# Optimization experiments

Hardware: AMD Instinct MI355X
Metric: run time of the kernel (lower is better)

The kernel has to match this reference:

```python
import jax, jax.numpy as jnp
import numpy as np

N = 32768      # nodes
E = 524288     # edges (avg degree 16)
G = 512        # graphs in batch
F_IN = 64      # one-hot node-label dim
H = 128        # hidden_dim
C = 2          # num_classes (NCI1)
BN_EPS = 1e-3  # keras BatchNormalization default epsilon


def setup_inputs() -> dict:
    key = jax.random.key(0)
    ks = jax.random.split(key, 32)
    d = {}
    d["x"] = jax.random.normal(ks[0], (N, F_IN), jnp.float32)
    d["edge_weight"] = jax.random.uniform(ks[1], (E,), jnp.float32)
    i = 2
    din = F_IN
    for l in range(5):
        d[f"W1_{l}"] = jax.random.normal(ks[i], (din, H), jnp.float32) / np.float32(np.sqrt(din)); i += 1
        d[f"b1_{l}"] = jnp.zeros((H,), jnp.float32)
        d[f"W2_{l}"] = jax.random.normal(ks[i], (H, H), jnp.float32) / np.float32(np.sqrt(H)); i += 1
        d[f"b2_{l}"] = jnp.zeros((H,), jnp.float32)
        din = H
    for j in (1, 2, 3):  # bn1, bn2, bn3 (bn0/bn4 unused in original call())
        d[f"g{j}"] = jnp.ones((H,), jnp.float32)
        d[f"be{j}"] = jnp.zeros((H,), jnp.float32)
        d[f"m{j}"] = jnp.zeros((H,), jnp.float32)
        d[f"v{j}"] = jnp.ones((H,), jnp.float32)
    d["Wm1"] = jax.random.normal(ks[i], (5 * H, 128), jnp.float32) / np.float32(np.sqrt(5 * H)); i += 1
    d["bm1"] = jnp.zeros((128,), jnp.float32)
    d["Wm2"] = jax.random.normal(ks[i], (128, C), jnp.float32) / np.float32(np.sqrt(128.0)); i += 1
    d["bm2"] = jnp.zeros((C,), jnp.float32)
    d["edge_index"] = jax.random.randint(ks[i], (2, E), 0, N, dtype=jnp.int32); i += 1
    d["node_graph_index"] = jnp.sort(jax.random.randint(ks[i], (N,), 0, G, dtype=jnp.int32))
    return d


def reference(x, edge_weight,
              W1_0, b1_0, W2_0, b2_0,
              W1_1, b1_1, W2_1, b2_1,
              W1_2, b1_2, W2_2, b2_2,
              W1_3, b1_3, W2_3, b2_3,
              W1_4, b1_4, W2_4, b2_4,
              g1, be1, m1, v1,
              g2, be2, m2, v2,
              g3, be3, m3, v3,
              Wm1, bm1, Wm2, bm2,
              edge_index, node_graph_index):
    src, dst = edge_index[0], edge_index[1]

    def gin(h, W1, b1, W2, b2):
        # GIN with eps=0: h' = MLP(h + sum_{j in N(i)} w_ij * h_j)
        msg = h[dst] * edge_weight[:, None]              # [E, d]
        agg = jax.ops.segment_sum(msg, src, num_segments=N)
        h2 = h + agg
        return jax.nn.relu(h2 @ W1 + b1) @ W2 + b2

    def bn(h, g, be, m, v):  # inference-mode batchnorm
        return (h - m) * jax.lax.rsqrt(v + BN_EPS) * g + be

    h1 = gin(x, W1_0, b1_0, W2_0, b2_0)
    h2 = gin(bn(h1, g1, be1, m1, v1), W1_1, b1_1, W2_1, b2_1)
    h3 = gin(bn(h2, g1, be1, m1, v1), W1_2, b1_2, W2_2, b2_2)  # bn1 reused, as in source
    h4 = gin(bn(h3, g2, be2, m2, v2), W1_3, b1_3, W2_3, b2_3)
    h5 = gin(bn(h4, g3, be3, m3, v3), W1_4, b1_4, W2_4, b2_4)
    h5 = bn(h5, g3, be3, m3, v3)                                # bn3 reused, as in source

    pool = lambda h: jax.ops.segment_sum(h, node_graph_index, num_segments=G)
    hg = jnp.concatenate([pool(h1), pool(h2), pool(h3), pool(h4), pool(h5)], axis=-1)  # [G, 5H]
    # readout MLP (dropout inactive at inference)
    return jax.nn.relu(hg @ Wm1 + bm1) @ Wm2 + bm2  # [G, C]
```

## Files before the change

### kernel.cpp

```cpp
#include <hip/hip_runtime.h>
#include <hip/hip_bf16.h>

#define NN 32768
#define EE 524288
#define GG 512
#define CAP 48

typedef __bf16 bf16x8 __attribute__((ext_vector_type(8)));
typedef float  f32x4  __attribute__((ext_vector_type(4)));
typedef float  f32x2  __attribute__((ext_vector_type(2)));

#define F8_ENC 0.25f
#define F8_DEC 4.0f

static __device__ __forceinline__ float bf2f(unsigned short u) {
    union { unsigned int i; float f; } v; v.i = ((unsigned int)u) << 16; return v.f;
}
static __device__ __forceinline__ unsigned short f2bf(float f) {
    __bf16 b = (__bf16)f;
    return __builtin_bit_cast(unsigned short, b);
}
static __device__ __forceinline__ unsigned int pk2(float a, float b) {
    return (unsigned int)f2bf(a) | ((unsigned int)f2bf(b) << 16);
}
static __device__ __forceinline__ void fmaV4(float* a, float w, uint2 hv) {
    a[0] += w * bf2f((unsigned short)(hv.x & 0xffff));
    a[1] += w * bf2f((unsigned short)(hv.x >> 16));
    a[2] += w * bf2f((unsigned short)(hv.y & 0xffff));
    a[3] += w * bf2f((unsigned short)(hv.y >> 16));
}
static __device__ __forceinline__ void fmaV8f8(float* a, float w, uint2 hv) {
    f32x2 p;
    p = __builtin_amdgcn_cvt_pk_f32_fp8((int)hv.x, false); a[0] += w * p[0]; a[1] += w * p[1];
    p = __builtin_amdgcn_cvt_pk_f32_fp8((int)hv.x, true);  a[2] += w * p[0]; a[3] += w * p[1];
    p = __builtin_amdgcn_cvt_pk_f32_fp8((int)hv.y, false); a[4] += w * p[0]; a[5] += w * p[1];
    p = __builtin_amdgcn_cvt_pk_f32_fp8((int)hv.y, true);  a[6] += w * p[0]; a[7] += w * p[1];
}

struct WJob { const float* in; unsigned short* out; int K; };
struct WJobs { WJob j[10]; };

__global__ __launch_bounds__(256) void build_kernel(WJobs jobs,
                                                    const int* __restrict__ src,
                                                    const int* __restrict__ dst,
                                                    const float* __restrict__ w,
                                                    int* __restrict__ cnt,
                                                    unsigned int* __restrict__ csr,
                                                    const float* __restrict__ x,
                                                    unsigned short* __restrict__ xb) {
    if (blockIdx.x < 2048) {
        int e = blockIdx.x * 256 + threadIdx.x;
        int s = src[e];
        int slot = atomicAdd(&cnt[s], 1);
        if (slot < CAP)
            csr[(size_t)s * CAP + slot] = (unsigned int)dst[e] | ((unsigned int)f2bf(w[e]) << 16);
    } else if (blockIdx.x < 2088) {
        int b = blockIdx.x - 2048;
        WJob jb = jobs.j[b >> 2];
        int quarter = b & 3;
        int per = jb.K * 128 / 4;
        for (int idx = quarter * per + threadIdx.x; idx < (quarter + 1) * per; idx += 256) {
            int k = idx >> 7, c = idx & 127;
            jb.out[c * jb.K + k] = f2bf(jb.in[idx]);
        }
    } else {
        int base = (blockIdx.x - 2088) * 4096 + threadIdx.x;
        #pragma unroll
        for (int k = 0; k < 16; ++k) {
            int idx = base + k * 256;
            xb[idx] = f2bf(x[idx]);
        }
    }
}

template<bool FIRST>
__global__ __launch_bounds__(256, 8) void agg_kernel(
        const unsigned short* __restrict__ h_in,
        const unsigned char* __restrict__ h8_in,
        const int* __restrict__ cnt,
        const unsigned int* __restrict__ csr,
        unsigned short* __restrict__ A1g) {

    constexpr int CH = FIRST ? 4 : 8;

    int tid = threadIdx.x;
    int wave = tid >> 6, lane = tid & 63;
    int i4 = lane >> 4;
    int half = (lane >> 3) & 1;
    int sub8 = lane & 7;
    int gbase = lane & 56;
    int r = wave * 4 + i4;
    int node = blockIdx.x * 16 + r;
    int nb = blockIdx.x * 16 + wave * 4;

    int d0 = min(cnt[nb], CAP), d1 = min(cnt[nb + 1], CAP);
    int d2 = min(cnt[nb + 2], CAP), d3 = min(cnt[nb + 3], CAP);
    int deg = (i4 == 0) ? d0 : (i4 == 1) ? d1 : (i4 == 2) ? d2 : d3;
    int md = max(max(d0, d1), max(d2, d3));
    int mc = (md + 7) >> 3;
    size_t ebase = (size_t)node * CAP;
    int off = half * 8 + sub8;

    unsigned int ev[6];
    #pragma unroll
    for (int c = 0; c < 6; ++c) {
        int p = c * 8 + sub8;
        unsigned int e2 = 0;
        if (p < deg) e2 = csr[ebase + p];
        ev[c] = e2;
    }

    float acc[CH];
    #pragma unroll
    for (int c = 0; c < CH; ++c) acc[c] = 0.f;

    const uint2* hp = FIRST ? (const uint2*)h_in : (const uint2*)h8_in;

    uint2 pre[4]; float wv[4];
    #pragma unroll
    for (int k = 0; k < 4; ++k) {
        unsigned int e2 = (unsigned int)__shfl((int)ev[0], gbase | k);
        wv[k] = bf2f((unsigned short)(e2 >> 16));
        pre[k] = hp[(size_t)(e2 & 0xffffu) * 16 + off];
    }
    #pragma unroll
    for (int c = 0; c < 6; ++c) {
        if (c >= mc) break;
        #pragma unroll
        for (int j = 0; j < 8; ++j) {
            int t = c * 8 + j;
            if constexpr (FIRST) fmaV4(acc, wv[t & 3], pre[t & 3]);
            else                 fmaV8f8(acc, wv[t & 3], pre[t & 3]);
            int tn = t + 4, cn = tn >> 3, jn = tn & 7;
            if (cn < 6) {
                unsigned int e2 = (unsigned int)__shfl((int)ev[cn], gbase | jn);
                wv[t & 3] = bf2f((unsigned short)(e2 >> 16));
                pre[t & 3] = hp[(size_t)(e2 & 0xffffu) * 16 + off];
            }
        }
    }

    if constexpr (FIRST) {
        uint2 selfv = ((const uint2*)h_in)[(size_t)node * 16 + off];
        acc[0] += bf2f((unsigned short)(selfv.x & 0xffff));
        acc[1] += bf2f((unsigned short)(selfv.x >> 16));
        acc[2] += bf2f((unsigned short)(selfv.y & 0xffff));
        acc[3] += bf2f((unsigned short)(selfv.y >> 16));
        *(uint2*)(A1g + (size_t)node * 64 + off * 4) =
            make_uint2(pk2(acc[0], acc[1]), pk2(acc[2], acc[3]));
    } else {
        #pragma unroll
        for (int i = 0; i < 8; ++i) acc[i] *= F8_DEC;
        uint4 selfv = ((const uint4*)h_in)[(size_t)node * 16 + off];
        acc[0] += bf2f((unsigned short)(selfv.x & 0xffff));
        acc[1] += bf2f((unsigned short)(selfv.x >> 16));
        acc[2] += bf2f((unsigned short)(selfv.y & 0xffff));
        acc[3] += bf2f((unsigned short)(selfv.y >> 16));
        acc[4] += bf2f((unsigned short)(selfv.z & 0xffff));
        acc[5] += bf2f((unsigned short)(selfv.z >> 16));
        acc[6] += bf2f((unsigned short)(selfv.w & 0xffff));
        acc[7] += bf2f((unsigned short)(selfv.w >> 16));
        *(uint4*)(A1g + (size_t)node * 128 + off * 8) =
            make_uint4(pk2(acc[0], acc[1]), pk2(acc[2], acc[3]),
                       pk2(acc[4], acc[5]), pk2(acc[6], acc[7]));
    }
}

template<bool FIRST, bool LAST>
__global__ __launch_bounds__(256) void mlp_kernel(
        const unsigned short* __restrict__ A1g,
        const unsigned short* __restrict__ W1t,
        const float* __restrict__ b1,
        const unsigned short* __restrict__ W2t,
        const float* __restrict__ b2,
        const float* __restrict__ g, const float* __restrict__ be,
        const float* __restrict__ m, const float* __restrict__ v,
        const int* __restrict__ gidx,
        unsigned short* __restrict__ h_out,
        unsigned char* __restrict__ h8_out,
        float* __restrict__ pools, int col_off) {

    constexpr int K1 = FIRST ? 64 : 128;
    constexpr int KS1 = K1 / 32;

    __shared__ unsigned int smem[2176];
    __shared__ float sscale[128], sshift[128];
    __shared__ int sgid[16];

    unsigned int* A1 = smem;
    unsigned int* T  = smem + 16 * 68;
    float* OUT = (float*)smem;

    int tid = threadIdx.x;
    int wave = tid >> 6, lane = tid & 63;
    int mrow = lane & 15, quad = lane >> 4;

    if (tid < 128) {
        float sc = g[tid] * rsqrtf(v[tid] + 1e-3f);
        sscale[tid] = sc;
        sshift[tid] = be[tid] - m[tid] * sc;
    } else if (tid < 144) {
        sgid[tid - 128] = gidx[blockIdx.x * 16 + (tid - 128)];
    }

    unsigned short* A1s = (unsigned short*)A1;
    if constexpr (FIRST) {
        if (tid < 128) {
            int row = tid >> 3, grp = tid & 7;
            *(uint4*)(A1s + row * 136 + grp * 8) =
                *(const uint4*)(A1g + (size_t)(blockIdx.x * 16 + row) * 64 + grp * 8);
        }
    } else {
        int row = tid >> 4, grp = tid & 15;
        *(uint4*)(A1s + row * 136 + grp * 8) =
            *(const uint4*)(A1g + (size_t)(blockIdx.x * 16 + row) * 128 + grp * 8);
    }
    __syncthreads();

    unsigned short* Ts = (unsigned short*)T;

    bf16x8 af[KS1];
    #pragma unroll
    for (int kk = 0; kk < KS1; ++kk)
        af[kk] = *(const bf16x8*)(A1s + mrow * 136 + kk * 32 + quad * 8);

    f32x4 acc1v[2];
    #pragma unroll
    for (int c = 0; c < 2; ++c) acc1v[c] = (f32x4){0.f, 0.f, 0.f, 0.f};
    #pragma unroll
    for (int c = 0; c < 2; ++c) {
        const bf16x8* Brow = (const bf16x8*)(W1t + (size_t)(wave * 32 + c * 16 + mrow) * K1);
        #pragma unroll
        for (int kk = 0; kk < KS1; ++kk)
            acc1v[c] = __builtin_amdgcn_mfma_f32_16x16x32_bf16(af[kk], Brow[kk * 4 + quad], acc1v[c], 0, 0, 0);
    }
    #pragma unroll
    for (int c = 0; c < 2; ++c) {
        int ocol = wave * 32 + c * 16 + mrow;
        float bv = b1[ocol];
        #pragma unroll
        for (int r = 0; r < 4; ++r)
            Ts[(quad * 4 + r) * 136 + ocol] = f2bf(fmaxf(acc1v[c][r] + bv, 0.f));
    }
    __syncthreads();

    bf16x8 a2f[4];
    #pragma unroll
    for (int kk = 0; kk < 4; ++kk)
        a2f[kk] = *(const bf16x8*)(Ts + mrow * 136 + kk * 32 + quad * 8);
    f32x4 acc2v[2];
    #pragma unroll
    for (int c = 0; c < 2; ++c) acc2v[c] = (f32x4){0.f, 0.f, 0.f, 0.f};
    #pragma unroll
    for (int c = 0; c < 2; ++c) {
        const bf16x8* Brow = (const bf16x8*)(W2t + (size_t)(wave * 32 + c * 16 + mrow) * 128);
        #pragma unroll
        for (int kk = 0; kk < 4; ++kk)
            acc2v[c] = __builtin_amdgcn_mfma_f32_16x16x32_bf16(a2f[kk], Brow[kk * 4 + quad], acc2v[c], 0, 0, 0);
    }
    __syncthreads();

    #pragma unroll
    for (int c = 0; c < 2; ++c) {
        int ocol = wave * 32 + c * 16 + mrow;
        float bv = b2[ocol];
        #pragma unroll
        for (int r = 0; r < 4; ++r)
            OUT[(quad * 4 + r) * 132 + ocol] = acc2v[c][r] + bv;
    }
    __syncthreads();

    if (!LAST) {
        int row = tid >> 4, q = tid & 15;
        const float* Op = OUT + row * 132 + q * 8;
        float o[8];
        #pragma unroll
        for (int i = 0; i < 8; ++i) {
            int c = q * 8 + i;
            o[i] = Op[i] * sscale[c] + sshift[c];
        }
        size_t rowbase = (size_t)(blockIdx.x * 16 + row);
        *(uint4*)(h_out + rowbase * 128 + q * 8) =
            make_uint4(pk2(o[0], o[1]), pk2(o[2], o[3]),
                       pk2(o[4], o[5]), pk2(o[6], o[7]));
        int w0 = __builtin_amdgcn_cvt_pk_fp8_f32(o[0] * F8_ENC, o[1] * F8_ENC, 0, false);
        w0 = __builtin_amdgcn_cvt_pk_fp8_f32(o[2] * F8_ENC, o[3] * F8_ENC, w0, true);
        int w1 = __builtin_amdgcn_cvt_pk_fp8_f32(o[4] * F8_ENC, o[5] * F8_ENC, 0, false);
        w1 = __builtin_amdgcn_cvt_pk_fp8_f32(o[6] * F8_ENC, o[7] * F8_ENC, w1, true);
        *(uint2*)(h8_out + rowbase * 128 + q * 8) =
            make_uint2((unsigned int)w0, (unsigned int)w1);
    }

    {
        int col = tid & 127, half = tid >> 7;
        float sc = LAST ? sscale[col] : 1.f;
        float sh = LAST ? sshift[col] : 0.f;
        float accp = 0.f;
        int cur = sgid[half * 8];
        for (int r = half * 8; r < half * 8 + 8; ++r) {
            int gi = sgid[r];
            if (gi != cur) {
                atomicAdd(&pools[(size_t)cur * 640 + col_off + col], accp);
                accp = 0.f;
                cur = gi;
            }
            float val = OUT[r * 132 + col];
            accp += LAST ? (val * sc + sh) : val;
        }
        atomicAdd(&pools[(size_t)cur * 640 + col_off + col], accp);
    }
}

__global__ __launch_bounds__(128) void readout(const float* __restrict__ pools,
                                               const float* __restrict__ Wm1,
                                               const float* __restrict__ bm1,
                                               const float* __restrict__ Wm2,
                                               const float* __restrict__ bm2,
                                               float* __restrict__ out) {
    __shared__ float row[640];
    __shared__ float partial[4];
    int gb = blockIdx.x;
    for (int k = threadIdx.x; k < 640; k += 128) row[k] = pools[(size_t)gb * 640 + k];
    __syncthreads();
    int j = threadIdx.x;
    float acc = bm1[j];
    for (int k = 0; k < 640; ++k) acc += row[k] * Wm1[(size_t)k * 128 + j];
    acc = fmaxf(acc, 0.f);
    float p0 = acc * Wm2[j * 2], p1 = acc * Wm2[j * 2 + 1];
    #pragma unroll
    for (int off = 32; off; off >>= 1) { p0 += __shfl_down(p0, off); p1 += __shfl_down(p1, off); }
    int wave = j >> 6;
    if ((j & 63) == 0) { partial[wave * 2] = p0; partial[wave * 2 + 1] = p1; }
    __syncthreads();
    if (j == 0) {
        out[gb * 2]     = bm2[0] + partial[0] + partial[2];
        out[gb * 2 + 1] = bm2[1] + partial[1] + partial[3];
    }
}

extern "C" void kernel_launch(void* const* d_in, const int* in_sizes, int n_in,
                              void* d_out, int out_size, void* d_ws, size_t ws_size,
                              hipStream_t stream) {
    const float* x  = (const float*)d_in[0];
    const float* ew = (const float*)d_in[1];
    const float *W1[5], *b1[5], *W2[5], *b2[5];
    for (int l = 0; l < 5; ++l) {
        W1[l] = (const float*)d_in[2 + 4 * l];
        b1[l] = (const float*)d_in[3 + 4 * l];
        W2[l] = (const float*)d_in[4 + 4 * l];
        b2[l] = (const float*)d_in[5 + 4 * l];
    }
    const float *bg[3], *bb[3], *bm[3], *bv[3];
    for (int j = 0; j < 3; ++j) {
        bg[j] = (const float*)d_in[22 + 4 * j];
        bb[j] = (const float*)d_in[23 + 4 * j];
        bm[j] = (const float*)d_in[24 + 4 * j];
        bv[j] = (const float*)d_in[25 + 4 * j];
    }
    const float* Wm1 = (const float*)d_in[34];
    const float* bm1 = (const float*)d_in[35];
    const float* Wm2 = (const float*)d_in[36];
    const float* bm2 = (const float*)d_in[37];
    const int* edge_index = (const int*)d_in[38];
    const int* src = edge_index;
    const int* dst = edge_index + EE;
    const int* gidx = (const int*)d_in[39];

    char* p = (char*)d_ws;
    auto alloc = [&](size_t bytes) -> void* {
        void* r = (void*)p;
        p += (bytes + 255) & ~(size_t)255;
        return r;
    };
    unsigned int* csr  = (unsigned int*)alloc((size_t)NN * CAP * 4);
    int* cnt           = (int*)alloc(NN * 4);
    unsigned short* xb = (unsigned short*)alloc((size_t)NN * 64 * 2);
    unsigned short* hA = (unsigned short*)alloc((size_t)NN * 128 * 2);
    unsigned short* hB = (unsigned short*)alloc((size_t)NN * 128 * 2);
    unsigned char* h8A = (unsigned char*)alloc((size_t)NN * 128);
    unsigned char* h8B = (unsigned char*)alloc((size_t)NN * 128);
    unsigned short* A1g = (unsigned short*)alloc((size_t)NN * 128 * 2);
    float* pools = (float*)alloc((size_t)GG * 640 * 4);
    unsigned short* W1t[5], *W2t[5];
    for (int l = 0; l < 5; ++l) {
        W1t[l] = (unsigned short*)alloc((size_t)128 * 128 * 2);
        W2t[l] = (unsigned short*)alloc((size_t)128 * 128 * 2);
    }

    hipMemsetAsync(cnt, 0, NN * 4, stream);
    hipMemsetAsync(pools, 0, (size_t)GG * 640 * 4, stream);

    WJobs jobs;
    for (int l = 0; l < 5; ++l) {
        jobs.j[2 * l]     = WJob{W1[l], W1t[l], (l == 0) ? 64 : 128};
        jobs.j[2 * l + 1] = WJob{W2[l], W2t[l], 128};
    }
    build_kernel<<<2048 + 40 + 512, 256, 0, stream>>>(jobs, src, dst, ew, cnt, csr, x, xb);

    const int bnsel[5] = {0, 0, 1, 2, 2};

    agg_kernel<true><<<NN / 16, 256, 0, stream>>>(xb, (const unsigned char*)nullptr, cnt, csr, A1g);
    mlp_kernel<true, false><<<NN / 16, 256, 0, stream>>>(
        A1g, W1t[0], b1[0], W2t[0], b2[0],
        bg[0], bb[0], bm[0], bv[0], gidx, hA, h8A, pools, 0);

    const unsigned short* hin = hA;
    unsigned short* hout = hB;
    const unsigned char* h8in = h8A;
    unsigned char* h8out = h8B;
    for (int l = 1; l < 5; ++l) {
        int s = bnsel[l];
        agg_kernel<false><<<NN / 16, 256, 0, stream>>>(hin, h8in, cnt, csr, A1g);
        if (l < 4) {
            mlp_kernel<false, false><<<NN / 16, 256, 0, stream>>>(
                A1g, W1t[l], b1[l], W2t[l], b2[l],
                bg[s], bb[s], bm[s], bv[s], gidx, hout, h8out, pools, l * 128);
        } else {
            mlp_kernel<false, true><<<NN / 16, 256, 0, stream>>>(
                A1g, W1t[l], b1[l], W2t[l], b2[l],
                bg[s], bb[s], bm[s], bv[s], gidx, hout, h8out, pools, l * 128);
        }
        unsigned short* tmp = (unsigned short*)hin;
        hin = hout;
        hout = tmp;
        unsigned char* tmp8 = (unsigned char*)h8in;
        h8in = h8out;
        h8out = tmp8;
    }

    readout<<<GG, 128, 0, stream>>>(pools, Wm1, bm1, Wm2, bm2, (float*)d_out);
}
```

Baseline: 342.9 us.

## Fuse neighbor aggregation into per-layer MLP kernel and split readout reduction

Merges the separate aggregation and MLP kernels into one layer kernel. The aggregated rows now go straight into shared memory instead of round-tripping through a global A1 buffer, which removes one launch per layer. The gather prefetch depth grows from 4 to 8 outstanding neighbor loads, and prefetching now stops at the real chunk count. The readout kernel splits the 640-long dot product across two thread halves. In exchange, the fused kernel uses more registers and shared memory, since OUT is now a separate buffer, which may lower occupancy under the 8-block launch bound.

```diff
diff --git a/kernel.cpp b/kernel.cpp
--- a/kernel.cpp
+++ b/kernel.cpp
@@ -73,102 +73,12 @@
     }
 }
 
-template<bool FIRST>
-__global__ __launch_bounds__(256, 8) void agg_kernel(
+template<bool FIRST, bool LAST>
+__global__ __launch_bounds__(256, 8) void layer_kernel(
         const unsigned short* __restrict__ h_in,
         const unsigned char* __restrict__ h8_in,
         const int* __restrict__ cnt,
         const unsigned int* __restrict__ csr,
-        unsigned short* __restrict__ A1g) {
-
-    constexpr int CH = FIRST ? 4 : 8;
-
-    int tid = threadIdx.x;
-    int wave = tid >> 6, lane = tid & 63;
-    int i4 = lane >> 4;
-    int half = (lane >> 3) & 1;
-    int sub8 = lane & 7;
-    int gbase = lane & 56;
-    int r = wave * 4 + i4;
-    int node = blockIdx.x * 16 + r;
-    int nb = blockIdx.x * 16 + wave * 4;
-
-    int d0 = min(cnt[nb], CAP), d1 = min(cnt[nb + 1], CAP);
-    int d2 = min(cnt[nb + 2], CAP), d3 = min(cnt[nb + 3], CAP);
-    int deg = (i4 == 0) ? d0 : (i4 == 1) ? d1 : (i4 == 2) ? d2 : d3;
-    int md = max(max(d0, d1), max(d2, d3));
-    int mc = (md + 7) >> 3;
-    size_t ebase = (size_t)node * CAP;
-    int off = half * 8 + sub8;
-
-    unsigned int ev[6];
-    #pragma unroll
-    for (int c = 0; c < 6; ++c) {
-        int p = c * 8 + sub8;
-        unsigned int e2 = 0;
-        if (p < deg) e2 = csr[ebase + p];
-        ev[c] = e2;
-    }
-
-    float acc[CH];
-    #pragma unroll
-    for (int c = 0; c < CH; ++c) acc[c] = 0.f;
-
-    const uint2* hp = FIRST ? (const uint2*)h_in : (const uint2*)h8_in;
-
-    uint2 pre[4]; float wv[4];
-    #pragma unroll
-    for (int k = 0; k < 4; ++k) {
-        unsigned int e2 = (unsigned int)__shfl((int)ev[0], gbase | k);
-        wv[k] = bf2f((unsigned short)(e2 >> 16));
-        pre[k] = hp[(size_t)(e2 & 0xffffu) * 16 + off];
-    }
-    #pragma unroll
-    for (int c = 0; c < 6; ++c) {
-        if (c >= mc) break;
-        #pragma unroll
-        for (int j = 0; j < 8; ++j) {
-            int t = c * 8 + j;
-            if constexpr (FIRST) fmaV4(acc, wv[t & 3], pre[t & 3]);
-            else                 fmaV8f8(acc, wv[t & 3], pre[t & 3]);
-            int tn = t + 4, cn = tn >> 3, jn = tn & 7;
-            if (cn < 6) {
-                unsigned int e2 = (unsigned int)__shfl((int)ev[cn], gbase | jn);
-                wv[t & 3] = bf2f((unsigned short)(e2 >> 16));
-                pre[t & 3] = hp[(size_t)(e2 & 0xffffu) * 16 + off];
-            }
-        }
-    }
-
-    if constexpr (FIRST) {
-        uint2 selfv = ((const uint2*)h_in)[(size_t)node * 16 + off];
-        acc[0] += bf2f((unsigned short)(selfv.x & 0xffff));
-        acc[1] += bf2f((unsigned short)(selfv.x >> 16));
-        acc[2] += bf2f((unsigned short)(selfv.y & 0xffff));
-        acc[3] += bf2f((unsigned short)(selfv.y >> 16));
-        *(uint2*)(A1g + (size_t)node * 64 + off * 4) =
-            make_uint2(pk2(acc[0], acc[1]), pk2(acc[2], acc[3]));
-    } else {
-        #pragma unroll
-        for (int i = 0; i < 8; ++i) acc[i] *= F8_DEC;
-        uint4 selfv = ((const uint4*)h_in)[(size_t)node * 16 + off];
-        acc[0] += bf2f((unsigned short)(selfv.x & 0xffff));
-        acc[1] += bf2f((unsigned short)(selfv.x >> 16));
-        acc[2] += bf2f((unsigned short)(selfv.y & 0xffff));
-        acc[3] += bf2f((unsigned short)(selfv.y >> 16));
-        acc[4] += bf2f((unsigned short)(selfv.z & 0xffff));
-        acc[5] += bf2f((unsigned short)(selfv.z >> 16));
-        acc[6] += bf2f((unsigned short)(selfv.w & 0xffff));
-        acc[7] += bf2f((unsigned short)(selfv.w >> 16));
-        *(uint4*)(A1g + (size_t)node * 128 + off * 8) =
-            make_uint4(pk2(acc[0], acc[1]), pk2(acc[2], acc[3]),
-                       pk2(acc[4], acc[5]), pk2(acc[6], acc[7]));
-    }
-}
-
-template<bool FIRST, bool LAST>
-__global__ __launch_bounds__(256) void mlp_kernel(
-        const unsigned short* __restrict__ A1g,
         const unsigned short* __restrict__ W1t,
         const float* __restrict__ b1,
         const unsigned short* __restrict__ W2t,
@@ -182,14 +92,15 @@
 
     constexpr int K1 = FIRST ? 64 : 128;
     constexpr int KS1 = K1 / 32;
-
-    __shared__ unsigned int smem[2176];
+    constexpr int CH = FIRST ? 4 : 8;
+
+    __shared__ unsigned int smem[16 * 68 * 2];
+    __shared__ float OUT[16 * 132];
     __shared__ float sscale[128], sshift[128];
     __shared__ int sgid[16];
 
     unsigned int* A1 = smem;
     unsigned int* T  = smem + 16 * 68;
-    float* OUT = (float*)smem;
 
     int tid = threadIdx.x;
     int wave = tid >> 6, lane = tid & 63;
@@ -203,20 +114,90 @@
         sgid[tid - 128] = gidx[blockIdx.x * 16 + (tid - 128)];
     }
 
-    unsigned short* A1s = (unsigned short*)A1;
-    if constexpr (FIRST) {
-        if (tid < 128) {
-            int row = tid >> 3, grp = tid & 7;
-            *(uint4*)(A1s + row * 136 + grp * 8) =
-                *(const uint4*)(A1g + (size_t)(blockIdx.x * 16 + row) * 64 + grp * 8);
-        }
-    } else {
-        int row = tid >> 4, grp = tid & 15;
-        *(uint4*)(A1s + row * 136 + grp * 8) =
-            *(const uint4*)(A1g + (size_t)(blockIdx.x * 16 + row) * 128 + grp * 8);
-    }
-    __syncthreads();
-
+    {
+        int i4 = lane >> 4;
+        int half = (lane >> 3) & 1;
+        int sub8 = lane & 7;
+        int gbase = lane & 56;
+        int r = wave * 4 + i4;
+        int node = blockIdx.x * 16 + r;
+        int nb = blockIdx.x * 16 + wave * 4;
+
+        int d0 = min(cnt[nb], CAP),     d1 = min(cnt[nb + 1], CAP);
+        int d2 = min(cnt[nb + 2], CAP), d3 = min(cnt[nb + 3], CAP);
+        int deg = (i4 == 0) ? d0 : (i4 == 1) ? d1 : (i4 == 2) ? d2 : d3;
+        int md = max(max(d0, d1), max(d2, d3));
+        int mc = (md + 7) >> 3;
+        size_t ebase = (size_t)node * CAP;
+        int off = half * 8 + sub8;
+
+        unsigned int ev[6];
+        #pragma unroll
+        for (int c = 0; c < 6; ++c) {
+            int p = c * 8 + sub8;
+            unsigned int e2 = 0;
+            if (p < deg) e2 = csr[ebase + p];
+            ev[c] = e2;
+        }
+
+        float acc[CH];
+        #pragma unroll
+        for (int c = 0; c < CH; ++c) acc[c] = 0.f;
+
+        const uint2* hp = FIRST ? (const uint2*)h_in : (const uint2*)h8_in;
+
+        uint2 pre[8]; float wv[8];
+        #pragma unroll
+        for (int k = 0; k < 8; ++k) {
+            unsigned int e2 = (unsigned int)__shfl((int)ev[0], gbase | k);
+            wv[k] = bf2f((unsigned short)(e2 >> 16));
+            pre[k] = hp[(size_t)(e2 & 0xffffu) * 16 + off];
+        }
+        #pragma unroll
+        for (int c = 0; c < 6; ++c) {
+            if (c >= mc) break;
+            #pragma unroll
+            for (int j = 0; j < 8; ++j) {
+                int t = c * 8 + j;
+                if constexpr (FIRST) fmaV4(acc, wv[t & 7], pre[t & 7]);
+                else                 fmaV8f8(acc, wv[t & 7], pre[t & 7]);
+                int tn = t + 8, cn = tn >> 3, jn = tn & 7;
+                if (cn < mc) {
+                    unsigned int e2 = (unsigned int)__shfl((int)ev[cn], gbase | jn);
+                    wv[t & 7] = bf2f((unsigned short)(e2 >> 16));
+                    pre[t & 7] = hp[(size_t)(e2 & 0xffffu) * 16 + off];
+                }
+            }
+        }
+
+        if constexpr (FIRST) {
+            uint2 selfv = ((const uint2*)h_in)[(size_t)node * 16 + off];
+            acc[0] += bf2f((unsigned short)(selfv.x & 0xffff));
+            acc[1] += bf2f((unsigned short)(selfv.x >> 16));
+            acc[2] += bf2f((unsigned short)(selfv.y & 0xffff));
+            acc[3] += bf2f((unsigned short)(selfv.y >> 16));
+            *(uint2*)(A1 + r * 68 + half * 16 + sub8 * 2) =
+                make_uint2(pk2(acc[0], acc[1]), pk2(acc[2], acc[3]));
+        } else {
+            #pragma unroll
+            for (int i = 0; i < 8; ++i) acc[i] *= F8_DEC;
+            uint4 selfv = ((const uint4*)h_in)[(size_t)node * 16 + off];
+            acc[0] += bf2f((unsigned short)(selfv.x & 0xffff));
+            acc[1] += bf2f((unsigned short)(selfv.x >> 16));
+            acc[2] += bf2f((unsigned short)(selfv.y & 0xffff));
+            acc[3] += bf2f((unsigned short)(selfv.y >> 16));
+            acc[4] += bf2f((unsigned short)(selfv.z & 0xffff));
+            acc[5] += bf2f((unsigned short)(selfv.z >> 16));
+            acc[6] += bf2f((unsigned short)(selfv.w & 0xffff));
+            acc[7] += bf2f((unsigned short)(selfv.w >> 16));
+            *(uint4*)(A1 + r * 68 + half * 32 + sub8 * 4) =
+                make_uint4(pk2(acc[0], acc[1]), pk2(acc[2], acc[3]),
+                           pk2(acc[4], acc[5]), pk2(acc[6], acc[7]));
+        }
+    }
+    __syncthreads();
+
+    const unsigned short* A1s = (const unsigned short*)A1;
     unsigned short* Ts = (unsigned short*)T;
 
     bf16x8 af[KS1];
@@ -258,8 +239,6 @@
         for (int kk = 0; kk < 4; ++kk)
             acc2v[c] = __builtin_amdgcn_mfma_f32_16x16x32_bf16(a2f[kk], Brow[kk * 4 + quad], acc2v[c], 0, 0, 0);
     }
-    __syncthreads();
-
     #pragma unroll
     for (int c = 0; c < 2; ++c) {
         int ocol = wave * 32 + c * 16 + mrow;
@@ -311,30 +290,38 @@
     }
 }
 
-__global__ __launch_bounds__(128) void readout(const float* __restrict__ pools,
+__global__ __launch_bounds__(256) void readout(const float* __restrict__ pools,
                                                const float* __restrict__ Wm1,
                                                const float* __restrict__ bm1,
                                                const float* __restrict__ Wm2,
                                                const float* __restrict__ bm2,
                                                float* __restrict__ out) {
     __shared__ float row[640];
-    __shared__ float partial[4];
+    __shared__ float part[264];
     int gb = blockIdx.x;
-    for (int k = threadIdx.x; k < 640; k += 128) row[k] = pools[(size_t)gb * 640 + k];
-    __syncthreads();
-    int j = threadIdx.x;
-    float acc = bm1[j];
-    for (int k = 0; k < 640; ++k) acc += row[k] * Wm1[(size_t)k * 128 + j];
-    acc = fmaxf(acc, 0.f);
-    float p0 = acc * Wm2[j * 2], p1 = acc * Wm2[j * 2 + 1];
-    #pragma unroll
-    for (int off = 32; off; off >>= 1) { p0 += __shfl_down(p0, off); p1 += __shfl_down(p1, off); }
-    int wave = j >> 6;
-    if ((j & 63) == 0) { partial[wave * 2] = p0; partial[wave * 2 + 1] = p1; }
-    __syncthreads();
-    if (j == 0) {
-        out[gb * 2]     = bm2[0] + partial[0] + partial[2];
-        out[gb * 2 + 1] = bm2[1] + partial[1] + partial[3];
+    int tid = threadIdx.x;
+    for (int k = tid; k < 640; k += 256) row[k] = pools[(size_t)gb * 640 + k];
+    __syncthreads();
+    int j = tid & 127, hh = tid >> 7;
+    float acc = 0.f;
+    const float* Wp = Wm1 + (size_t)(hh * 320) * 128 + j;
+    #pragma unroll 4
+    for (int k = 0; k < 320; ++k) acc += row[hh * 320 + k] * Wp[(size_t)k * 128];
+    part[tid] = acc;
+    __syncthreads();
+    if (tid < 128) {
+        float full = part[tid] + part[tid + 128] + bm1[tid];
+        full = fmaxf(full, 0.f);
+        float p0 = full * Wm2[tid * 2], p1 = full * Wm2[tid * 2 + 1];
+        #pragma unroll
+        for (int off = 32; off; off >>= 1) { p0 += __shfl_down(p0, off); p1 += __shfl_down(p1, off); }
+        int wv = tid >> 6;
+        if ((tid & 63) == 0) { part[256 + wv * 2] = p0; part[257 + wv * 2] = p1; }
+    }
+    __syncthreads();
+    if (tid == 0) {
+        out[gb * 2]     = bm2[0] + part[256] + part[258];
+        out[gb * 2 + 1] = bm2[1] + part[257] + part[259];
     }
 }
 
@@ -379,7 +366,6 @@
     unsigned short* hB = (unsigned short*)alloc((size_t)NN * 128 * 2);
     unsigned char* h8A = (unsigned char*)alloc((size_t)NN * 128);
     unsigned char* h8B = (unsigned char*)alloc((size_t)NN * 128);
-    unsigned short* A1g = (unsigned short*)alloc((size_t)NN * 128 * 2);
     float* pools = (float*)alloc((size_t)GG * 640 * 4);
     unsigned short* W1t[5], *W2t[5];
     for (int l = 0; l < 5; ++l) {
@@ -399,9 +385,8 @@
 
     const int bnsel[5] = {0, 0, 1, 2, 2};
 
-    agg_kernel<true><<<NN / 16, 256, 0, stream>>>(xb, (const unsigned char*)nullptr, cnt, csr, A1g);
-    mlp_kernel<true, false><<<NN / 16, 256, 0, stream>>>(
-        A1g, W1t[0], b1[0], W2t[0], b2[0],
+    layer_kernel<true, false><<<NN / 16, 256, 0, stream>>>(
+        xb, (const unsigned char*)nullptr, cnt, csr, W1t[0], b1[0], W2t[0], b2[0],
         bg[0], bb[0], bm[0], bv[0], gidx, hA, h8A, pools, 0);
 
     const unsigned short* hin = hA;
@@ -410,14 +395,13 @@
     unsigned char* h8out = h8B;
     for (int l = 1; l < 5; ++l) {
         int s = bnsel[l];
-        agg_kernel<false><<<NN / 16, 256, 0, stream>>>(hin, h8in, cnt, csr, A1g);
         if (l < 4) {
-            mlp_kernel<false, false><<<NN / 16, 256, 0, stream>>>(
-                A1g, W1t[l], b1[l], W2t[l], b2[l],
+            layer_kernel<false, false><<<NN / 16, 256, 0, stream>>>(
+                hin, h8in, cnt, csr, W1t[l], b1[l], W2t[l], b2[l],
                 bg[s], bb[s], bm[s], bv[s], gidx, hout, h8out, pools, l * 128);
         } else {
-            mlp_kernel<false, true><<<NN / 16, 256, 0, stream>>>(
-                A1g, W1t[l], b1[l], W2t[l], b2[l],
+            layer_kernel<false, true><<<NN / 16, 256, 0, stream>>>(
+                hin, h8in, cnt, csr, W1t[l], b1[l], W2t[l], b2[l],
                 bg[s], bb[s], bm[s], bv[s], gidx, hout, h8out, pools, l * 128);
         }
         unsigned short* tmp = (unsigned short*)hin;
@@ -428,5 +412,5 @@
         h8out = tmp8;
     }
 
-    readout<<<GG, 128, 0, stream>>>(pools, Wm1, bm1, Wm2, bm2, (float*)d_out);
-}
+    readout<<<GG, 256, 0, stream>>>(pools, Wm1, bm1, Wm2, bm2, (float*)d_out);
+}
```

After: 429.2 us. +25.2%, slower.
